# Kernel optimization log

Measured on AMD Instinct MI355X. Metric: run time of the kernel, lower is better.

The kernel has to match this reference:

```python
import jax, jax.numpy as jnp
import numpy as np

SR = 22050
FLOOR = 60.0
BPO = 12

def _interp_linear(p, T):
    # torch F.interpolate(mode='linear', align_corners=False)
    S = p.shape[0]
    x = np.clip((np.arange(T, dtype=np.float64) + 0.5) * (S / T) - 0.5, 0.0, S - 1)
    i0 = np.floor(x).astype(np.int64)
    i1 = np.minimum(i0 + 1, S - 1)
    f = (x - i0).astype(np.float32)
    return p[i0] * (1.0 - f) + p[i1] * f

def _hann(n):
    # torch.hann_window(n, periodic=True)
    if n <= 0:
        return np.zeros((0,), np.float32)
    return (0.5 - 0.5 * np.cos(2.0 * np.pi * np.arange(n) / n)).astype(np.float32)

def _find_voiced(f0, i):
    sub = f0[i:]
    if sub.size == 0:
        return None
    flag = (sub > 0.0).astype(np.int64)
    flag[0] = 0
    if not flag.any():
        return None
    rel = int(flag.argmax())
    after = flag[rel:]
    z = np.nonzero(after == 0)[0]
    run = int(z[0]) if z.size else int(after.size)
    return i + rel, i + rel + run

def _l2n(v):
    # F.normalize(dim=-1), eps=1e-12
    return v / np.maximum(np.linalg.norm(v, axis=-1, keepdims=True), 1e-12)

def _find_peak(signal, f0, i, right_dir):
    w = int(SR / max(float(f0[i]), FLOOR))
    s = max(i - w // 2, 0)
    if right_dir:
        cand_l, cand_r = int(i + 0.3 * w), int(i + 0.75 * w)
    else:
        cand_l, cand_r = max(int(i - 1.75 * w), 0), max(int(i - 1.3 * w), 0)
    if cand_l == cand_r or len(signal) - cand_l < w:
        return w, -1.0, i, 0.0
    seg = np.lib.stride_tricks.sliding_window_view(signal[cand_l:cand_r + w], w)
    corr = _l2n(seg) @ _l2n(signal[s:s + w])
    r = int(corr.argmax())
    return w, float(corr[r]), i + (r + cand_l) - s, float(np.abs(seg[r]).max())

def _find_allpeaks(signal, f0):
    gp = float(np.abs(signal).max())
    added_right, i, peaks = -1e308, 0, []
    while True:
        voiced = _find_voiced(f0, i)
        if voiced is None:
            break
        left, right = voiced
        middle = (left + right) // 2
        w = int(SR / float(f0[middle]))
        s = max(middle - w // 2, 0)
        seg = signal[s:s + w]
        mn, imn = float(seg.min()), int(seg.argmin())
        mx, imx = float(seg.max()), int(seg.argmax())
        i = middle if mn == mx else s + (imn if abs(mn) > abs(mx) else imx)
        backup = i
        while True:
            w, corr, i, peak = _find_peak(signal, f0, i, False)
            if corr == -1.0:
                i -= w
            if i < left:
                if corr > 0.7 and peak > 0.023333 * gp and i - added_right > 0.8 * w:
                    peaks.append(i)
                break
            if corr > 0.3 and (peak == 0.0 or peak > 0.01 * gp):
                if i - added_right > 0.8 * w:
                    peaks.append(i)
        i = backup
        while True:
            w, corr, i, peak = _find_peak(signal, f0, i, True)
            if corr == -1.0:
                i += w
            if i >= right:
                if corr > 0.7 and peak > 0.023333 * gp:
                    peaks.append(i)
                    added_right = i
                break
            if corr > 0.3 and (peak == 0.0 or peak > 0.01 * gp):
                peaks.append(i)
                added_right = i
        i = right
    if not peaks:
        return None
    return np.clip(np.array(sorted(peaks), dtype=np.int64), 0, len(signal) - 1)

def _psola_plan(signal, pitch, peaks):
    # Returns list of (dst_idx, src_idx, window) overlap-add ops plus tail index.
    T = len(signal)
    idx = np.arange(T)
    max_w = 1.25 * SR / float(pitch[pitch > 0].min())
    ops, i = [], 0
    while i < T:
        voiced = _find_voiced(pitch, i)
        if voiced is None:
            break
        left_v, right_v = voiced
        if i < left_v:
            ops.append((idx[i:left_v], idx[i:left_v], _hann(left_v - i)))
        while left_v < right_v:
            p = int(np.abs(peaks - left_v).argmin())
            period = int(SR / max(float(pitch[left_v]), FLOOR))
            left_w = right_w = period // 2
            if p > 0 and peaks[p] - peaks[p - 1] <= max_w:
                left_w = min(int(peaks[p] - peaks[p - 1]), left_w)
            if p < len(peaks) - 1 and peaks[p + 1] - peaks[p] <= max_w:
                right_w = min(int(peaks[p + 1] - peaks[p]), right_w)
            left_i = max(int(peaks[p]) - left_w, 0)
            right_i = int(peaks[p]) + right_w
            ival = (right_i - left_i) // 2
            if ival <= 0:  # safety guard; unreachable for speech-range pitch
                break
            win = _hann(ival * 2)
            seglen = min(len(idx[left_v - ival:left_v + ival]), len(idx[left_i:left_i + ival * 2]))
            dst = idx[left_v - ival:left_v - ival + seglen]
            src = idx[left_i:left_i + seglen]
            L = min(len(dst), len(src), seglen)
            ops.append((dst[:L], src[:L], win[:L]))
            left_v += ival * 2
        i = right_v
    return ops, i

def _pitch_shift_plan(snd, pitch, steps, pitch_range):
    if not (pitch > 1e-05).any():
        return None
    f0 = _interp_linear(pitch, len(snd))
    peaks = _find_allpeaks(snd, f0)
    if peaks is None:
        return None
    v = np.sort(pitch[pitch > 0.0])
    median = float(v[(len(v) - 1) // 2])  # torch lower median
    factor = 2.0 ** (steps / BPO)
    f0, median = f0 * factor, median * factor
    f0 = np.where(f0 > 0.0, median + (f0 - median) * pitch_range, 0.0).astype(np.float32)
    return _psola_plan(snd, f0, peaks)

def setup_inputs():
    key = jax.random.key(0)
    T, S = 661500, 3000
    t = np.arange(S)
    base = (170.0 + 40.0 * np.sin(2.0 * np.pi * t / 400.0)).astype(np.float32)
    voiced = (t % 75) >= 15  # alternating unvoiced/voiced runs
    pitch = np.where(voiced, base, 0.0).astype(np.float32)
    f0 = _interp_linear(pitch, T)
    phase = 2.0 * np.pi * np.cumsum(f0.astype(np.float64)) / SR
    noise = np.asarray(jax.random.normal(key, (T,)), np.float32)
    snd = np.where(f0 > 0.0, 0.55 * np.sin(phase) + 0.25 * np.sin(2 * phase) + 0.1 * np.sin(3 * phase), 0.0)
    snd = np.clip(snd + 0.02 * noise, -1.0, 1.0).astype(np.float32)
    return {"snd": jnp.asarray(snd), "pitch": jnp.asarray(pitch), "steps": 3, "pitch_range": jnp.float32(1.0)}

def reference(snd, pitch, steps, pitch_range):
    snd_np = np.asarray(snd, np.float32)
    pitch_np = np.asarray(pitch, np.float32)
    plan = _pitch_shift_plan(snd_np, pitch_np, int(steps), float(pitch_range))
    if plan is None:
        return jnp.asarray(snd_np)
    ops, tail = plan
    out = np.zeros_like(snd_np)
    for dst, src, win in ops:
        out[dst] += win * snd_np[src]
    out[tail:] = snd_np[tail:]
    return jnp.asarray(out)
```

## Files before the change

kernel.cpp:

```cpp
#include <hip/hip_runtime.h>
#include <cfloat>
#include <climits>
#include <math.h>

#define SRATE 22050.0
#define WMAX 512
#define RCAP 128
#define LCR 256
#define RCR 512
#define SCAP 16384
#define OPR 256
#define MSL 3072
#define NTW 256
#define NTM 1024
#define PCAP 8192
#define FCAP 16384
#define PSTG 4096
#define SNDW 15872
#define RPW 136
#define APPLYB 2048
#define TAILB 1024


__global__ __launch_bounds__(256) void kstats(const float* __restrict__ pitch, int S, unsigned* scal) {
  __shared__ float sp[MSL];
  __shared__ int sc[256];
  __shared__ int sa[256];
  __shared__ unsigned hist[256];
  __shared__ unsigned sprefix, smask;
  __shared__ int srank;
  int tid = threadIdx.x;
  if (tid < 64) scal[tid] = (tid == 1) ? 0x7f800000u : 0u;
  bool lds = (S <= MSL);
  int c = 0, a = 0;
  for (int j = tid; j < S; j += 256) {
    float v = pitch[j];
    if (lds) sp[j] = v;
    if (v > 0.0f) c++;
    if (v > 1e-05f) a = 1;
  }
  sc[tid] = c; sa[tid] = a; __syncthreads();
  for (int st = 128; st; st >>= 1) {
    if (tid < st) { sc[tid] += sc[tid + st]; sa[tid] |= sa[tid + st]; }
    __syncthreads();
  }
  int n = sc[0];
  if (tid == 0) { scal[15] = (unsigned)n; scal[3] = (unsigned)sa[0]; }
  if (n == 0) return;
  if (tid == 0) { sprefix = 0u; smask = 0u; srank = (n - 1) >> 1; }
  __syncthreads();
  for (int shift = 24; shift >= 0; shift -= 8) {
    hist[tid] = 0u;
    __syncthreads();
    unsigned pfx = sprefix, msk = smask;
    for (int q = tid; q < S; q += 256) {
      float v = lds ? sp[q] : pitch[q];
      if (v > 0.0f) {
        unsigned u = __float_as_uint(v);
        if ((u & msk) == pfx) atomicAdd(&hist[(u >> shift) & 255u], 1u);
      }
    }
    __syncthreads();
    if (tid == 0) {
      int r = srank;
      unsigned b = 0;
      for (;;) { unsigned cc = hist[b]; if (r < (int)cc) break; r -= (int)cc; b++; }
      srank = r;
      sprefix = pfx | (b << shift);
      smask = msk | (0xFFu << shift);
    }
    __syncthreads();
  }
  if (tid == 0) scal[2] = sprefix;
}

__device__ __forceinline__ float interp1(const float* __restrict__ pitch, int S, double r, int t) {
  double x = ((double)t + 0.5) * r - 0.5;
  if (x < 0.0) x = 0.0;
  double sm1 = (double)(S - 1);
  if (x > sm1) x = sm1;
  double fl = floor(x);
  int i0 = (int)fl;
  int i1 = i0 + 1; if (i1 > S - 1) i1 = S - 1;
  float f = (float)(x - fl);
  return __fadd_rn(__fmul_rn(pitch[i0], __fsub_rn(1.0f, f)), __fmul_rn(pitch[i1], f));
}

__global__ __launch_bounds__(256) void kprep(const float* __restrict__ pitch, int S, int T,
                                             const float* __restrict__ snd, unsigned* scal,
                                             const int* __restrict__ steps_p, const float* __restrict__ pr_p,
                                             int* __restrict__ pd, int* __restrict__ w0,
                                             int* s0l, int* e0l, int* s1l, int* e1l) {
  __shared__ float smax[256];
  __shared__ unsigned smin[256];
  float med = __uint_as_float(scal[2]);
  double factor = exp2((double)steps_p[0] / 12.0);
  float fac32 = (float)factor;
  float m32 = (float)((double)med * factor);
  float pr32 = pr_p[0];
  double r = (double)S / (double)T;
  float amax = 0.0f;
  unsigned lmin = 0x7f800000u;
  int lane = threadIdx.x & 63;
  int stride = gridDim.x * blockDim.x;
  for (int t = blockIdx.x * blockDim.x + threadIdx.x; t < T; t += stride) {
    float v = interp1(pitch, S, r, t);
    float v1 = __fmul_rn(v, fac32);
    float vs = 0.0f;
    if (v1 > 0.0f) vs = __fadd_rn(m32, __fmul_rn(__fsub_rn(v1, m32), pr32));
    if (t == 1) { scal[16] = __float_as_uint(v); scal[17] = __float_as_uint(vs); }
    { double fd = (double)vs; if (fd < 60.0) fd = 60.0; pd[t] = (int)(SRATE / fd); }
    { double fi = (double)v; if (fi < 60.0) fi = 60.0;
      int ww = (int)(SRATE / fi); if (ww < 1) ww = 1; if (ww > WMAX - 1) ww = WMAX - 1;
      w0[t] = ww; }
    if (vs > 0.0f) { unsigned b = __float_as_uint(vs); if (b < lmin) lmin = b; }
    float a = fabsf(snd[t]); if (a > amax) amax = a;
    bool pv = false, pv1 = false;
    float upv = __shfl_up(v, 1, 64);
    if (t > 0) {
      float pvv = (lane == 0) ? interp1(pitch, S, r, t - 1) : upv;
      pv = pvv > 0.0f;
      float pm1 = __fmul_rn(pvv, fac32);
      float pvs = 0.0f;
      if (pm1 > 0.0f) pvs = __fadd_rn(m32, __fmul_rn(__fsub_rn(pm1, m32), pr32));
      pv1 = pvs > 0.0f;
    }
    bool cv = v > 0.0f, cv1 = vs > 0.0f;
    if (cv && (t == 0 || !pv))  { unsigned k = atomicAdd(scal + 8, 1u);  if (k < RCAP) s0l[k] = t; }
    if (!cv && t > 0 && pv)     { unsigned k = atomicAdd(scal + 9, 1u);  if (k < RCAP) e0l[k] = t; }
    if (cv1 && (t == 0 || !pv1)){ unsigned k = atomicAdd(scal + 10, 1u); if (k < RCAP) s1l[k] = t; }
    if (!cv1 && t > 0 && pv1)   { unsigned k = atomicAdd(scal + 11, 1u); if (k < RCAP) e1l[k] = t; }
  }
  smax[threadIdx.x] = amax; smin[threadIdx.x] = lmin; __syncthreads();
  for (int st = 128; st; st >>= 1) {
    if (threadIdx.x < st) {
      float o = smax[threadIdx.x + st]; if (o > smax[threadIdx.x]) smax[threadIdx.x] = o;
      unsigned u = smin[threadIdx.x + st]; if (u < smin[threadIdx.x]) smin[threadIdx.x] = u;
    }
    __syncthreads();
  }
  if (threadIdx.x == 0) {
    atomicMax(scal + 0, __float_as_uint(smax[0]));
    atomicMin(scal + 1, smin[0]);
  }
}

__device__ void ranksort(int* a, int n, int tid, int* tmp) {
  int v = 0, rk = 0;
  if (tid < n) {
    v = a[tid];
    for (int q = 0; q < n; q++) if (a[q] < v) rk++;
  }
  __syncthreads();
  if (tid < n) tmp[rk] = v;
  __syncthreads();
  if (tid < n) a[tid] = tmp[tid];
  __syncthreads();
}

__device__ int pair_regions_lds(float f1, int T, int* sl, int ns, int* el, int ne, int* L, int* R) {
  int b = 0;
  if (ns > 0 && sl[0] == 0) {
    if (T > 1 && f1 > 0.0f) sl[0] = 1;
    else b = 1;
  }
  int m = 0, j = 0;
  for (int k = b; k < ns; k++) {
    int Lv = sl[k];
    while (j < ne && el[j] <= Lv) j++;
    int Rv = (j < ne) ? el[j] : T;
    if (m < RCAP) { L[m] = Lv; R[m] = Rv; m++; }
  }
  return m;
}

__global__ __launch_bounds__(128) void kregsort2(int T, unsigned* scal,
                                                 const int* __restrict__ s0l, const int* __restrict__ e0l,
                                                 const int* __restrict__ s1l, const int* __restrict__ e1l,
                                                 int* r0L, int* r0R, int* r1L, int* r1R) {
  __shared__ int A[RCAP], B[RCAP], C[RCAP], D[RCAP];
  __shared__ int tmp[RCAP];
  __shared__ int LA[RCAP], RA[RCAP];
  int tid = threadIdx.x;
  int ns0 = min((int)scal[8], RCAP), ne0 = min((int)scal[9], RCAP);
  int ns1 = min((int)scal[10], RCAP), ne1 = min((int)scal[11], RCAP);
  if (tid < ns0) A[tid] = s0l[tid];
  if (tid < ne0) B[tid] = e0l[tid];
  if (tid < ns1) C[tid] = s1l[tid];
  if (tid < ne1) D[tid] = e1l[tid];
  __syncthreads();
  ranksort(A, ns0, tid, tmp);
  ranksort(B, ne0, tid, tmp);
  ranksort(C, ns1, tid, tmp);
  ranksort(D, ne1, tid, tmp);
  float f0_1 = (T > 1) ? __uint_as_float(scal[16]) : 0.0f;
  float f0s_1 = (T > 1) ? __uint_as_float(scal[17]) : 0.0f;
  __shared__ int m0s, m1s;
  if (tid == 0) {
    m0s = pair_regions_lds(f0_1, T, A, ns0, B, ne0, LA, RA);
  }
  __syncthreads();
  if (tid < m0s) { r0L[tid] = LA[tid]; r0R[tid] = RA[tid]; }
  __syncthreads();
  if (tid == 0) {
    m1s = pair_regions_lds(f0s_1, T, C, ns1, D, ne1, LA, RA);
  }
  __syncthreads();
  if (tid < m1s) { r1L[tid] = LA[tid]; r1R[tid] = RA[tid]; }
  if (tid == 0) { scal[12] = (unsigned)m0s; scal[13] = (unsigned)m1s; }
}

struct FPRes { int w; int i; float corr; float peak; };
struct FPG { int w, s, cl, nw, rlen; bool ok; };

__device__ __forceinline__ FPG fp_geom(int T, int i, int w, bool right_dir) {
  FPG g;
  int s = i - w / 2; if (s < 0) s = 0;
  int cl, cr;
  if (right_dir) {
    cl = (int)((double)i + 0.3 * (double)w);
    cr = (int)((double)i + 0.75 * (double)w);
  } else {
    double al = (double)i - 1.75 * (double)w;
    double bl = (double)i - 1.3 * (double)w;
    cl = (int)al; if (cl < 0) cl = 0;
    cr = (int)bl; if (cr < 0) cr = 0;
  }
  g.w = w; g.s = s; g.cl = cl;
  g.ok = !(cl == cr || T - cl < w);
  int nw = (((cr + w) < T ? (cr + w) : T)) - cl - w + 1;
  if (nw < 1) nw = 1;
  g.nw = nw;
  int rlen = T - s; if (rlen > w) rlen = w;
  g.rlen = rlen;
  return g;
}

template <bool L>
__device__ __forceinline__ FPRes fp_impl(const float* __restrict__ snd, const float* lsnd, int wb0,
                                         FPG g, int i, int tid,
                                         float (*refp)[RPW], double* sdd, float* swf, int* swi, float* swp) {
  FPRes res;
  int w = g.w, s = g.s, cl = g.cl, nw = g.nw, rlen = g.rlen;
  res.w = w;
  int lane = tid & 63, wv = tid >> 6;
  double part = 0.0;
  for (int k = tid; k < w; k += NTW) {
    float v = (k < rlen) ? (L ? lsnd[s + k - wb0] : snd[s + k]) : 0.0f;
    refp[k & 3][k >> 2] = v;
    part += (double)v * (double)v;
  }
  for (int off = 32; off; off >>= 1) part += __shfl_xor(part, off, 64);
  if (lane == 0) sdd[wv] = part;
  __syncthreads();
  double refden = sqrt(sdd[0] + sdd[1] + sdd[2] + sdd[3]);
  if (refden < 1e-12) refden = 1e-12;
  int gg = tid >> 2, sub = tid & 3;
  float bestv = -FLT_MAX; int bestr = INT_MAX; float bestp = 0.0f;
  for (int base = 0; base < nw; base += 64) {
    int r = base + gg;
    if (r < nw) {
      const float* seg = (L ? (lsnd + (cl - wb0)) : (snd + cl)) + r;
      const float* rrow = refp[sub];
      double d0 = 0.0, d1 = 0.0, n0 = 0.0, n1 = 0.0;
      float pkc = 0.0f;
      int k = sub, j = 0;
      for (; k + 12 < w; k += 16, j += 4) {
        float4 rv = *reinterpret_cast<const float4*>(rrow + j);
        float a0f = seg[k], a1f = seg[k + 4];
        pkc = fmaxf(pkc, fabsf(a0f));
        pkc = fmaxf(pkc, fabsf(a1f));
        double a0 = (double)a0f, a1 = (double)a1f;
        d0 += a0 * (double)rv.x; n0 += a0 * a0;
        d1 += a1 * (double)rv.y; n1 += a1 * a1;
        float a2f = seg[k + 8], a3f = seg[k + 12];
        pkc = fmaxf(pkc, fabsf(a2f));
        pkc = fmaxf(pkc, fabsf(a3f));
        double a2 = (double)a2f, a3 = (double)a3f;
        d0 += a2 * (double)rv.z; n0 += a2 * a2;
        d1 += a3 * (double)rv.w; n1 += a3 * a3;
      }
      for (; k + 4 < w; k += 8) {
        float a0f = seg[k], a1f = seg[k + 4];
        pkc = fmaxf(pkc, fabsf(a0f));
        pkc = fmaxf(pkc, fabsf(a1f));
        double a0 = (double)a0f, b0 = (double)refp[k & 3][k >> 2];
        double a1 = (double)a1f, b1 = (double)refp[(k + 4) & 3][(k + 4) >> 2];
        d0 += a0 * b0; n0 += a0 * a0;
        d1 += a1 * b1; n1 += a1 * a1;
      }
      for (; k < w; k += 4) {
        float af = seg[k];
        pkc = fmaxf(pkc, fabsf(af));
        double a = (double)af; d0 += a * (double)refp[k & 3][k >> 2]; n0 += a * a;
      }
      double dot = d0 + d1, nr2 = n0 + n1;
      dot += __shfl_xor(dot, 1, 64); nr2 += __shfl_xor(nr2, 1, 64);
      pkc = fmaxf(pkc, __shfl_xor(pkc, 1, 64));
      dot += __shfl_xor(dot, 2, 64); nr2 += __shfl_xor(nr2, 2, 64);
      pkc = fmaxf(pkc, __shfl_xor(pkc, 2, 64));
      if (sub == 0) {
        double den = sqrt(nr2); if (den < 1e-12) den = 1e-12;
        float c = (float)(dot / (den * refden));
        if (c > bestv) { bestv = c; bestr = r; bestp = pkc; }
      }
    }
  }
  for (int off = 32; off >= 4; off >>= 1) {
    float ov = __shfl_xor(bestv, off, 64);
    int orr = __shfl_xor(bestr, off, 64);
    float op = __shfl_xor(bestp, off, 64);
    if (ov > bestv || (ov == bestv && orr < bestr)) { bestv = ov; bestr = orr; bestp = op; }
  }
  if (lane == 0) { swf[wv] = bestv; swi[wv] = bestr; swp[wv] = bestp; }
  __syncthreads();
  float bv = swf[0]; int br = swi[0]; float bp = swp[0];
  for (int q = 1; q < 4; q++) {
    float ov = swf[q]; int orr = swi[q]; float op = swp[q];
    if (ov > bv || (ov == bv && orr < br)) { bv = ov; br = orr; bp = op; }
  }
  res.corr = bv;
  res.i = i + (br + cl) - s;
  res.peak = bp;
  return res;
}

__device__ __forceinline__ FPRes find_peak_block(const float* __restrict__ snd,
                                                 const float* lsnd, int wb0, int wb1, bool useW,
                                                 int T, int i, int wcur, bool right_dir, int tid,
                                                 float (*refp)[RPW], double* sdd,
                                                 float* swf, int* swi, float* swp) {
  FPG g = fp_geom(T, i, wcur, right_dir);
  if (!g.ok) { FPRes r; r.w = g.w; r.corr = -1.0f; r.i = i; r.peak = 0.0f; return r; }
  int lo_a = g.s < g.cl ? g.s : g.cl;
  int hi1 = g.s + g.w, hi2 = g.cl + g.nw + g.w;
  int hi_a = hi1 > hi2 ? hi1 : hi2;
  bool inW = useW && lo_a >= wb0 && hi_a <= wb1;
  if (inW) return fp_impl<true>(snd, lsnd, wb0, g, i, tid, refp, sdd, swf, swi, swp);
  return fp_impl<false>(snd, lsnd, wb0, g, i, tid, refp, sdd, swf, swi, swp);
}

__global__ __launch_bounds__(NTW) void kwalk(const float* __restrict__ snd,
                                             const float* __restrict__ pitch, int S,
                                             const int* __restrict__ w0,
                                             int T, const unsigned* scal,
                                             const int* __restrict__ r0L, const int* __restrict__ r0R,
                                             int2* __restrict__ lcand, int* __restrict__ lcnt,
                                             int* __restrict__ rpk, int* __restrict__ rcnt) {
  __shared__ float lsnd[SNDW];
  __shared__ short swtab[SNDW];
  __shared__ __align__(16) float refp[4][RPW];
  __shared__ double sdd[4];
  __shared__ float swf[8];
  __shared__ int swi[8];
  __shared__ float swp[4];
  __shared__ float spitch[PSTG];
  int tid = threadIdx.x;
  int lane = tid & 63, wv = tid >> 6;
  if (scal[3] == 0u) return;
  bool useL = (S <= PSTG);
  if (useL) { for (int k = tid; k < S; k += NTW) spitch[k] = pitch[k]; }
  __syncthreads();
  double rr = (double)S / (double)T;
  int nreg = (int)scal[12];
  float gp = __uint_as_float(scal[0]);
  for (int wid = blockIdx.x; wid < 2 * nreg; wid += gridDim.x) {
    int r = wid >> 1;
    bool rightdir = (wid & 1) != 0;
    int left = r0L[r], right = r0R[r];
    int middle = (left + right) >> 1;
    int wb0 = left - 1024; if (wb0 < 0) wb0 = 0;
    int wb1 = right + 1024; if (wb1 > T) wb1 = T;
    bool useW = (wb1 - wb0) <= SNDW;
    __syncthreads();
    if (useW) {
      for (int k = tid; k < wb1 - wb0; k += NTW) {
        lsnd[k] = snd[wb0 + k];
        swtab[k] = (short)w0[wb0 + k];
      }
    }
    __syncthreads();
    double fm = useL ? (double)interp1(spitch, S, rr, middle) : (double)interp1(pitch, S, rr, middle);
    double wd = SRATE / fm;
    long long wcap = 2LL * (long long)T;
    int w = (wd >= (double)wcap) ? (int)wcap : (int)wd;
    if (w < 1) w = 1;
    int s0 = middle - w / 2; if (s0 < 0) s0 = 0;
    int wlen = w; if (wlen > T - s0) wlen = T - s0;
    float lmn = FLT_MAX; int lmni = INT_MAX;
    float lmx = -FLT_MAX; int lmxi = INT_MAX;
    for (int k = tid; k < wlen; k += NTW) {
      int idx = s0 + k;
      float v = (useW && idx >= wb0 && idx < wb1) ? lsnd[idx - wb0] : snd[idx];
      if (v < lmn) { lmn = v; lmni = k; }
      if (v > lmx) { lmx = v; lmxi = k; }
    }
    for (int off = 32; off; off >>= 1) {
      float ov = __shfl_xor(lmn, off, 64); int oi = __shfl_xor(lmni, off, 64);
      if (ov < lmn || (ov == lmn && oi < lmni)) { lmn = ov; lmni = oi; }
      float ov2 = __shfl_xor(lmx, off, 64); int oi2 = __shfl_xor(lmxi, off, 64);
      if (ov2 > lmx || (ov2 == lmx && oi2 < lmxi)) { lmx = ov2; lmxi = oi2; }
    }
    if (lane == 0) { swf[wv] = lmn; swi[wv] = lmni; swf[4 + wv] = lmx; swi[4 + wv] = lmxi; }
    __syncthreads();
    float mn = swf[0]; int imn = swi[0];
    float mx = swf[4]; int imx = swi[4];
    for (int q = 1; q < 4; q++) {
      float ov = swf[q]; int oi = swi[q];
      if (ov < mn || (ov == mn && oi < imn)) { mn = ov; imn = oi; }
      float ov2 = swf[4 + q]; int oi2 = swi[4 + q];
      if (ov2 > mx || (ov2 == mx && oi2 < imx)) { mx = ov2; imx = oi2; }
    }
    __syncthreads();
    int i;
    if (mn == mx) i = middle;
    else i = s0 + ((fabsf(mn) > fabsf(mx)) ? imn : imx);
    if (!rightdir) {
      int nl = 0, guard = 0;
      for (;;) {
        if (++guard > 500000) break;
        int wcur;
        if (useW && i >= wb0 && i < wb1) wcur = (int)swtab[i - wb0];
        else {
          double fi = useL ? (double)interp1(spitch, S, rr, i) : (double)interp1(pitch, S, rr, i);
          if (fi < 60.0) fi = 60.0;
          int ww = (int)(SRATE / fi); if (ww < 1) ww = 1; if (ww > WMAX - 1) ww = WMAX - 1;
          wcur = ww;
        }
        FPRes p = find_peak_block(snd, lsnd, wb0, wb1, useW, T, i, wcur, false, tid,
                                  refp, sdd, swf, swi, swp);
        i = p.i;
        if (p.corr == -1.0f) i -= p.w;
        if (i < left) {
          if ((double)p.corr > 0.7 && (double)p.peak > 0.023333 * (double)gp) {
            if (nl < LCR) { if (tid == 0) lcand[r * LCR + nl] = make_int2(i, p.w); nl++; }
          }
          break;
        }
        if ((double)p.corr > 0.3 && (p.peak == 0.0f || (double)p.peak > 0.01 * (double)gp)) {
          if (nl < LCR) { if (tid == 0) lcand[r * LCR + nl] = make_int2(i, p.w); nl++; }
        }
      }
      if (tid == 0) lcnt[r] = nl;
    } else {
      int nr = 0, guard = 0;
      for (;;) {
        if (++guard > 500000) break;
        int wcur;
        if (useW && i >= wb0 && i < wb1) wcur = (int)swtab[i - wb0];
        else {
          double fi = useL ? (double)interp1(spitch, S, rr, i) : (double)interp1(pitch, S, rr, i);
          if (fi < 60.0) fi = 60.0;
          int ww = (int)(SRATE / fi); if (ww < 1) ww = 1; if (ww > WMAX - 1) ww = WMAX - 1;
          wcur = ww;
        }
        FPRes p = find_peak_block(snd, lsnd, wb0, wb1, useW, T, i, wcur, true, tid,
                                  refp, sdd, swf, swi, swp);
        i = p.i;
        if (p.corr == -1.0f) i += p.w;
        if (i >= right) {
          if ((double)p.corr > 0.7 && (double)p.peak > 0.023333 * (double)gp) {
            if (nr < RCR) { if (tid == 0) rpk[r * RCR + nr] = i; nr++; }
          }
          break;
        }
        if ((double)p.corr > 0.3 && (p.peak == 0.0f || (double)p.peak > 0.01 * (double)gp)) {
          if (nr < RCR) { if (tid == 0) rpk[r * RCR + nr] = i; nr++; }
        }
      }
      if (tid == 0) rcnt[r] = nr;
    }
  }
}

__global__ __launch_bounds__(NTM) void kmerge(int T, unsigned* scal,
                                              const int2* __restrict__ lcand, const int* __restrict__ lcnt,
                                              const int* __restrict__ rpk, const int* __restrict__ rcnt,
                                              int* __restrict__ peaks) {
  __shared__ long long arR[RCAP];
  __shared__ long long lastR[RCAP];
  __shared__ int rcs[RCAP];
  __shared__ int lcs[RCAP];
  __shared__ int klc[RCAP];
  __shared__ int off[RCAP + 1];
  __shared__ int sbuf[SCAP];
  __shared__ int unsorted;
  int tid = threadIdx.x;
  int lane = tid & 63, wv = tid >> 6;
  int nreg = (int)scal[12];
  if (scal[3] == 0u || nreg == 0) { if (tid == 0) scal[4] = 0u; return; }
  if (tid < nreg) {
    int rc = rcnt[tid];
    rcs[tid] = rc;
    lcs[tid] = lcnt[tid];
    lastR[tid] = (rc > 0) ? (long long)rpk[tid * RCR + rc - 1] : LLONG_MIN;
  }
  __syncthreads();
  if (tid == 0) {
    long long ar = -(1LL << 62);
    for (int r = 0; r < nreg; r++) { arR[r] = ar; if (rcs[r] > 0) ar = lastR[r]; }
  }
  __syncthreads();
  for (int r = wv; r < nreg; r += 16) {
    int n = lcs[r];
    long long ar = arR[r];
    int cnt = 0;
    for (int base = 0; base < n; base += 64) {
      int jp = base + lane;
      bool pred = false;
      if (jp < n) {
        int j = n - 1 - jp;
        int2 cd = lcand[r * LCR + j];
        pred = ((double)((long long)cd.x - ar) > 0.8 * (double)cd.y);
      }
      unsigned long long m = __ballot(pred);
      cnt += __popcll(m);
    }
    if (lane == 0) klc[r] = cnt;
  }
  __syncthreads();
  if (tid == 0) {
    int acc = 0;
    for (int r = 0; r < nreg; r++) { off[r] = acc; acc += klc[r] + rcs[r]; if (acc > SCAP) acc = SCAP; }
    off[nreg] = acc;
    scal[4] = (unsigned)acc;
    unsorted = 0;
  }
  __syncthreads();
  for (int r = wv; r < nreg; r += 16) {
    long long ar = arR[r];
    int n = lcs[r];
    int pos0 = off[r];
    for (int base = 0; base < n; base += 64) {
      int jp = base + lane;
      bool pred = false; int val = 0;
      if (jp < n) {
        int j = n - 1 - jp;
        int2 cd = lcand[r * LCR + j];
        if ((double)((long long)cd.x - ar) > 0.8 * (double)cd.y) { pred = true; val = cd.x; }
      }
      unsigned long long m = __ballot(pred);
      if (pred) {
        int pre = __popcll(m & ((1ull << lane) - 1ull));
        int pos = pos0 + pre;
        if (pos < SCAP) peaks[pos] = val;
      }
      pos0 += __popcll(m);
    }
    int rc = rcs[r];
    for (int j = lane; j < rc; j += 64) {
      int pos = pos0 + j;
      if (pos < SCAP) peaks[pos] = rpk[r * RCR + j];
    }
  }
  __syncthreads();
  int npk = off[nreg];
  if (npk > 1) {
    for (int k = tid; k < npk - 1; k += NTM) {
      if (peaks[k] > peaks[k + 1]) unsorted = 1;
    }
    __syncthreads();
    if (unsorted) {
      int n2 = 1; while (n2 < npk) n2 <<= 1;
      for (int k = tid; k < n2; k += NTM) sbuf[k] = (k < npk) ? peaks[k] : INT_MAX;
      __syncthreads();
      for (int kk = 2; kk <= n2; kk <<= 1) {
        for (int j = kk >> 1; j > 0; j >>= 1) {
          for (int idx = tid; idx < n2; idx += NTM) {
            int ixj = idx ^ j;
            if (ixj > idx) {
              int a = sbuf[idx], b = sbuf[ixj];
              bool up = ((idx & kk) == 0);
              if ((up && a > b) || (!up && a < b)) { sbuf[idx] = b; sbuf[ixj] = a; }
            }
          }
          __syncthreads();
        }
      }
      for (int k = tid; k < npk; k += NTM) peaks[k] = sbuf[k];
      __syncthreads();
    }
  }
  for (int k = tid; k < npk; k += NTM) { int v = peaks[k]; if (v < 0) v = 0; if (v > T - 1) v = T - 1; peaks[k] = v; }
}

__global__ __launch_bounds__(256) void kplan(const int* __restrict__ pd, int T, unsigned* scal,
                                             const int* __restrict__ peaks,
                                             const int* __restrict__ r1L, const int* __restrict__ r1R,
                                             int4* __restrict__ ops, int* __restrict__ opcnt) {
  __shared__ int sp[PCAP];
  __shared__ int ib[FCAP];
  int tid = threadIdx.x;
  int npk = (int)scal[4];
  int nreg = (int)scal[13];
  int r = (int)blockIdx.x;
  if (scal[3] == 0u || npk == 0) {
    if (r == 0 && tid == 0) { scal[6] = 0u; scal[14] = 0u; }
    return;
  }
  if (r == 0 && tid == 0) {
    scal[6] = (nreg > 0) ? (unsigned)r1R[nreg - 1] : 0u;
    scal[14] = (unsigned)nreg;
  }
  if (r >= nreg) return;
  int prev_right = (r == 0) ? 0 : r1R[r - 1];
  int left_v = r1L[r], right_v = r1R[r];
  int pl_n = npk < PCAP ? npk : PCAP;
  int pl4 = pl_n & ~3;
  for (int k = tid * 4; k < pl4; k += 1024) {
    int4 v = *reinterpret_cast<const int4*>(peaks + k);
    sp[k] = v.x; sp[k + 1] = v.y; sp[k + 2] = v.z; sp[k + 3] = v.w;
  }
  for (int k = pl4 + tid; k < pl_n; k += 256) sp[k] = peaks[k];
  int span = right_v - left_v;
  int fl_n = span < FCAP ? span : FCAP;
  const int* srcp = pd + left_v;
  int head = (4 - (left_v & 3)) & 3; if (head > fl_n) head = fl_n;
  for (int k = tid; k < head; k += 256) ib[k] = srcp[k];
  int rem4 = (fl_n - head) & ~3;
  for (int k = tid * 4; k < rem4; k += 1024) {
    int4 v = *reinterpret_cast<const int4*>(srcp + head + k);
    ib[head + k] = v.x; ib[head + k + 1] = v.y; ib[head + k + 2] = v.z; ib[head + k + 3] = v.w;
  }
  for (int k = head + rem4 + tid; k < fl_n; k += 256) ib[k] = srcp[k];
  __syncthreads();
  if (tid != 0) return;

  auto PRD = [&](int idx) -> int { return (idx < pl_n) ? sp[idx] : peaks[idx]; };

  double minpos = (double)__uint_as_float(scal[1]);
  double max_w = 1.25 * SRATE / minpos;
  int c = 0;
  if (prev_right < left_v) {
    ops[r * OPR + c] = make_int4(prev_right, prev_right, left_v - prev_right, left_v - prev_right);
    c++;
  }
  int lv = left_v, guard = 0;
  int lo = -1;
  int Pm2 = 0, Pm1 = 0, P0 = 0, P1 = 0;
  while (lv < right_v) {
    if (++guard > 500000) break;
    int fo = lv - left_v;
    int period = (fo < fl_n) ? ib[fo] : pd[lv];
    int x = lv;
    if (lo < 0) {
      int a = 0, b = npk;
      while (a < b) { int m = (a + b) >> 1; if (PRD(m) < x) a = m + 1; else b = m; }
      lo = a;
      Pm2 = (lo - 2 >= 0) ? PRD(lo - 2) : 0;
      Pm1 = (lo - 1 >= 0) ? PRD(lo - 1) : 0;
      P0  = (lo < npk) ? PRD(lo) : 0;
      P1  = (lo + 1 < npk) ? PRD(lo + 1) : 0;
    } else {
      while (lo < npk && P0 < x) {
        lo++;
        Pm2 = Pm1; Pm1 = P0; P0 = P1;
        P1 = (lo + 1 < npk) ? PRD(lo + 1) : 0;
      }
    }
    long long d0 = (lo > 0) ? (long long)x - (long long)Pm1 : LLONG_MAX;
    long long d1 = (lo < npk) ? (long long)P0 - (long long)x : LLONG_MAX;
    int p, Pp, Ppm1, Pp1;
    if (d0 <= d1) {
      p = lo - 1;
      int tv = Pm1;
      if (p > 0 && Pm2 == tv) {
        while (p > 0 && PRD(p - 1) == tv) p--;
        Pp = tv;
        Ppm1 = (p > 0) ? PRD(p - 1) : 0;
        Pp1 = (p < npk - 1) ? PRD(p + 1) : 0;
      } else {
        Pp = Pm1; Ppm1 = Pm2; Pp1 = P0;
      }
    } else {
      p = lo; Pp = P0; Ppm1 = Pm1; Pp1 = P1;
    }
    int lw = period >> 1, rw = period >> 1;
    if (p > 0) { long long gp_ = (long long)Pp - (long long)Ppm1; if ((double)gp_ <= max_w && gp_ < (long long)lw) lw = (int)gp_; }
    if (p < npk - 1) { long long gp_ = (long long)Pp1 - (long long)Pp; if ((double)gp_ <= max_w && gp_ < (long long)rw) rw = (int)gp_; }
    int left_i = Pp - lw; if (left_i < 0) left_i = 0;
    int right_i = Pp + rw;
    int ival = (right_i - left_i) >> 1;
    if (ival <= 0) break;
    int a0 = lv - ival;
    int len1 = 0;
    if (a0 >= 0) { int e = lv + ival; if (e > T) e = T; len1 = e - a0; if (len1 < 0) len1 = 0; }
    int e2 = left_i + 2 * ival; if (e2 > T) e2 = T;
    int len2 = e2 - left_i; if (len2 < 0) len2 = 0;
    int seglen = len1 < len2 ? len1 : len2;
    int len_dst = (a0 < 0) ? 0 : ((T - a0 < seglen) ? T - a0 : seglen);
    int len_src = (T - left_i < seglen) ? T - left_i : seglen;
    int L = seglen; if (len_dst < L) L = len_dst; if (len_src < L) L = len_src;
    if (L > 0 && c < OPR) { ops[r * OPR + c] = make_int4(a0, left_i, L, 2 * ival); c++; }
    lv += 2 * ival;
  }
  opcnt[r] = c;
}

__global__ __launch_bounds__(256) void kout(const float* __restrict__ snd, float* __restrict__ out,
                                            const unsigned* scal, const int4* __restrict__ ops,
                                            const int* __restrict__ opcnt, int T) {
  int tail = (int)scal[6];
  if (blockIdx.x < APPLYB) {
    int nreg = (int)scal[14];
    int total = nreg * OPR;
    for (int slot = blockIdx.x; slot < total; slot += APPLYB) {
      int r = slot / OPR, j = slot - r * OPR;
      if (j >= opcnt[r]) continue;
      int4 o = ops[r * OPR + j];
      double nn = (double)o.w;
      int kend = o.z;
      { int lim = tail - o.x; if (lim < 0) lim = 0; if (kend > lim) kend = lim; }
      for (int k = threadIdx.x; k < kend; k += blockDim.x) {
        double cph = (6.283185307179586 * (double)k) / nn;
        float wv = (float)(0.5 - 0.5 * cos(cph));
        atomicAdd(out + o.x + k, __fmul_rn(wv, snd[o.y + k]));
      }
    }
  } else {
    int b = blockIdx.x - APPLYB;
    int stride = TAILB * 256;
    for (int t = b * 256 + threadIdx.x; t < T; t += stride)
      if (t >= tail) out[t] = snd[t];
  }
}

extern "C" void kernel_launch(void* const* d_in, const int* in_sizes, int n_in,
                              void* d_out, int out_size, void* d_ws, size_t ws_size,
                              hipStream_t stream) {
  (void)n_in; (void)ws_size;
  int T = in_sizes[0];
  int S = in_sizes[1];
  const float* snd = (const float*)d_in[0];
  const float* pitch = (const float*)d_in[1];
  const int* steps = (const int*)d_in[2];
  const float* prange = (const float*)d_in[3];
  float* out = (float*)d_out;

  char* base = (char*)d_ws;
  size_t off = 0;
  auto alloc = [&](size_t bytes, size_t align) -> char* {
    off = (off + align - 1) & ~(align - 1);
    char* p = base + off;
    off += bytes;
    return p;
  };
  int* pd    = (int*)alloc((size_t)T * 4, 16);
  int* w0    = (int*)alloc((size_t)T * 4, 16);
  unsigned* scal = (unsigned*)alloc(256, 16);
  int* s0l = (int*)alloc(RCAP * 4, 4);
  int* e0l = (int*)alloc(RCAP * 4, 4);
  int* s1l = (int*)alloc(RCAP * 4, 4);
  int* e1l = (int*)alloc(RCAP * 4, 4);
  int* r0L = (int*)alloc(RCAP * 4, 4);
  int* r0R = (int*)alloc(RCAP * 4, 4);
  int* r1L = (int*)alloc(RCAP * 4, 4);
  int* r1R = (int*)alloc(RCAP * 4, 4);
  int* lcnt = (int*)alloc(RCAP * 4, 4);
  int* rcnt = (int*)alloc(RCAP * 4, 4);
  int* opcnt = (int*)alloc(RCAP * 4, 4);
  int2* lcand = (int2*)alloc((size_t)RCAP * LCR * 8, 8);
  int* rpk = (int*)alloc((size_t)RCAP * RCR * 4, 4);
  int* peaks = (int*)alloc((size_t)SCAP * 4, 16);
  int4* ops = (int4*)alloc((size_t)RCAP * OPR * 16, 16);

  hipMemsetAsync(d_out, 0, (size_t)out_size * sizeof(float), stream);
  kstats<<<1, 256, 0, stream>>>(pitch, S, scal);
  kprep<<<1024, 256, 0, stream>>>(pitch, S, T, snd, scal, steps, prange, pd, w0, s0l, e0l, s1l, e1l);
  kregsort2<<<1, 128, 0, stream>>>(T, scal, s0l, e0l, s1l, e1l, r0L, r0R, r1L, r1R);
  kwalk<<<256, NTW, 0, stream>>>(snd, pitch, S, w0, T, scal, r0L, r0R, lcand, lcnt, rpk, rcnt);
  kmerge<<<1, NTM, 0, stream>>>(T, scal, lcand, lcnt, rpk, rcnt, peaks);
  kplan<<<RCAP, 256, 0, stream>>>(pd, T, scal, peaks, r1L, r1R, ops, opcnt);
  kout<<<APPLYB + TAILB, 256, 0, stream>>>(snd, out, scal, ops, opcnt, T);
}
```

Baseline: 458.2 us.

## Fold region sort and peak merge into walk and plan kernels, dropping launches

Removes the single-block region-sort kernel and the single-block peak-merge kernel. Each kwalk block now redundantly sorts and pairs the voiced-region boundaries in LDS, and each kplan block redundantly rebuilds the merged, sorted peak list directly in its own shared memory instead of reading it from global. This cuts two serial kernel launches and their global round trips from a latency-bound pipeline. In exchange, every block repeats the sort/merge work, and kplan's shared-memory footprint grows, which may lower occupancy.

```diff
diff --git a/kernel.cpp b/kernel.cpp
--- a/kernel.cpp
+++ b/kernel.cpp
@@ -12,7 +12,6 @@
 #define OPR 256
 #define MSL 3072
 #define NTW 256
-#define NTM 1024
 #define PCAP 8192
 #define FCAP 16384
 #define PSTG 4096
@@ -174,42 +173,6 @@
   return m;
 }
 
-__global__ __launch_bounds__(128) void kregsort2(int T, unsigned* scal,
-                                                 const int* __restrict__ s0l, const int* __restrict__ e0l,
-                                                 const int* __restrict__ s1l, const int* __restrict__ e1l,
-                                                 int* r0L, int* r0R, int* r1L, int* r1R) {
-  __shared__ int A[RCAP], B[RCAP], C[RCAP], D[RCAP];
-  __shared__ int tmp[RCAP];
-  __shared__ int LA[RCAP], RA[RCAP];
-  int tid = threadIdx.x;
-  int ns0 = min((int)scal[8], RCAP), ne0 = min((int)scal[9], RCAP);
-  int ns1 = min((int)scal[10], RCAP), ne1 = min((int)scal[11], RCAP);
-  if (tid < ns0) A[tid] = s0l[tid];
-  if (tid < ne0) B[tid] = e0l[tid];
-  if (tid < ns1) C[tid] = s1l[tid];
-  if (tid < ne1) D[tid] = e1l[tid];
-  __syncthreads();
-  ranksort(A, ns0, tid, tmp);
-  ranksort(B, ne0, tid, tmp);
-  ranksort(C, ns1, tid, tmp);
-  ranksort(D, ne1, tid, tmp);
-  float f0_1 = (T > 1) ? __uint_as_float(scal[16]) : 0.0f;
-  float f0s_1 = (T > 1) ? __uint_as_float(scal[17]) : 0.0f;
-  __shared__ int m0s, m1s;
-  if (tid == 0) {
-    m0s = pair_regions_lds(f0_1, T, A, ns0, B, ne0, LA, RA);
-  }
-  __syncthreads();
-  if (tid < m0s) { r0L[tid] = LA[tid]; r0R[tid] = RA[tid]; }
-  __syncthreads();
-  if (tid == 0) {
-    m1s = pair_regions_lds(f0s_1, T, C, ns1, D, ne1, LA, RA);
-  }
-  __syncthreads();
-  if (tid < m1s) { r1L[tid] = LA[tid]; r1R[tid] = RA[tid]; }
-  if (tid == 0) { scal[12] = (unsigned)m0s; scal[13] = (unsigned)m1s; }
-}
-
 struct FPRes { int w; int i; float corr; float peak; };
 struct FPG { int w, s, cl, nw, rlen; bool ok; };
 
@@ -344,7 +307,7 @@
                                              const float* __restrict__ pitch, int S,
                                              const int* __restrict__ w0,
                                              int T, const unsigned* scal,
-                                             const int* __restrict__ r0L, const int* __restrict__ r0R,
+                                             const int* __restrict__ s0l, const int* __restrict__ e0l,
                                              int2* __restrict__ lcand, int* __restrict__ lcnt,
                                              int* __restrict__ rpk, int* __restrict__ rcnt) {
   __shared__ float lsnd[SNDW];
@@ -355,19 +318,29 @@
   __shared__ int swi[8];
   __shared__ float swp[4];
   __shared__ float spitch[PSTG];
+  __shared__ int rsA[RCAP], rsB[RCAP], rsT[RCAP], rLA[RCAP], rRA[RCAP];
+  __shared__ int m0sh;
   int tid = threadIdx.x;
   int lane = tid & 63, wv = tid >> 6;
   if (scal[3] == 0u) return;
+  int ns0 = min((int)scal[8], RCAP), ne0 = min((int)scal[9], RCAP);
+  if (tid < ns0) rsA[tid] = s0l[tid];
+  if (tid < ne0) rsB[tid] = e0l[tid];
   bool useL = (S <= PSTG);
   if (useL) { for (int k = tid; k < S; k += NTW) spitch[k] = pitch[k]; }
   __syncthreads();
+  ranksort(rsA, ns0, tid, rsT);
+  ranksort(rsB, ne0, tid, rsT);
+  float f0_1 = (T > 1) ? __uint_as_float(scal[16]) : 0.0f;
+  if (tid == 0) m0sh = pair_regions_lds(f0_1, T, rsA, ns0, rsB, ne0, rLA, rRA);
+  __syncthreads();
+  int nreg = m0sh;
   double rr = (double)S / (double)T;
-  int nreg = (int)scal[12];
   float gp = __uint_as_float(scal[0]);
   for (int wid = blockIdx.x; wid < 2 * nreg; wid += gridDim.x) {
     int r = wid >> 1;
     bool rightdir = (wid & 1) != 0;
-    int left = r0L[r], right = r0R[r];
+    int left = rLA[r], right = rRA[r];
     int middle = (left + right) >> 1;
     int wb0 = left - 1024; if (wb0 < 0) wb0 = 0;
     int wb1 = right + 1024; if (wb1 > T) wb1 = T;
@@ -473,145 +446,154 @@
   }
 }
 
-__global__ __launch_bounds__(NTM) void kmerge(int T, unsigned* scal,
-                                              const int2* __restrict__ lcand, const int* __restrict__ lcnt,
-                                              const int* __restrict__ rpk, const int* __restrict__ rcnt,
-                                              int* __restrict__ peaks) {
+__global__ __launch_bounds__(256) void kplan(const int* __restrict__ pd, int T, unsigned* scal,
+                                             const int2* __restrict__ lcand, const int* __restrict__ lcnt,
+                                             const int* __restrict__ rpk, const int* __restrict__ rcnt,
+                                             const int* __restrict__ s0l, const int* __restrict__ e0l,
+                                             const int* __restrict__ s1l, const int* __restrict__ e1l,
+                                             int4* __restrict__ ops, int* __restrict__ opcnt) {
+  __shared__ int sp[SCAP];
+  __shared__ int ib[FCAP];
+  __shared__ int rsA[RCAP], rsB[RCAP], rsT[RCAP], rLA[RCAP], rRA[RCAP];
   __shared__ long long arR[RCAP];
   __shared__ long long lastR[RCAP];
-  __shared__ int rcs[RCAP];
-  __shared__ int lcs[RCAP];
-  __shared__ int klc[RCAP];
-  __shared__ int off[RCAP + 1];
-  __shared__ int sbuf[SCAP];
-  __shared__ int unsorted;
+  __shared__ int rcs[RCAP], lcs[RCAP], klc[RCAP], off[RCAP + 1];
+  __shared__ int m0sh, m1sh, unsorted;
   int tid = threadIdx.x;
   int lane = tid & 63, wv = tid >> 6;
-  int nreg = (int)scal[12];
-  if (scal[3] == 0u || nreg == 0) { if (tid == 0) scal[4] = 0u; return; }
-  if (tid < nreg) {
-    int rc = rcnt[tid];
-    rcs[tid] = rc;
-    lcs[tid] = lcnt[tid];
-    lastR[tid] = (rc > 0) ? (long long)rpk[tid * RCR + rc - 1] : LLONG_MIN;
-  }
-  __syncthreads();
-  if (tid == 0) {
-    long long ar = -(1LL << 62);
-    for (int r = 0; r < nreg; r++) { arR[r] = ar; if (rcs[r] > 0) ar = lastR[r]; }
-  }
-  __syncthreads();
-  for (int r = wv; r < nreg; r += 16) {
-    int n = lcs[r];
-    long long ar = arR[r];
-    int cnt = 0;
-    for (int base = 0; base < n; base += 64) {
-      int jp = base + lane;
-      bool pred = false;
-      if (jp < n) {
-        int j = n - 1 - jp;
-        int2 cd = lcand[r * LCR + j];
-        pred = ((double)((long long)cd.x - ar) > 0.8 * (double)cd.y);
-      }
-      unsigned long long m = __ballot(pred);
-      cnt += __popcll(m);
-    }
-    if (lane == 0) klc[r] = cnt;
-  }
-  __syncthreads();
-  if (tid == 0) {
-    int acc = 0;
-    for (int r = 0; r < nreg; r++) { off[r] = acc; acc += klc[r] + rcs[r]; if (acc > SCAP) acc = SCAP; }
-    off[nreg] = acc;
-    scal[4] = (unsigned)acc;
-    unsorted = 0;
-  }
-  __syncthreads();
-  for (int r = wv; r < nreg; r += 16) {
-    long long ar = arR[r];
-    int n = lcs[r];
-    int pos0 = off[r];
-    for (int base = 0; base < n; base += 64) {
-      int jp = base + lane;
-      bool pred = false; int val = 0;
-      if (jp < n) {
-        int j = n - 1 - jp;
-        int2 cd = lcand[r * LCR + j];
-        if ((double)((long long)cd.x - ar) > 0.8 * (double)cd.y) { pred = true; val = cd.x; }
-      }
-      unsigned long long m = __ballot(pred);
-      if (pred) {
-        int pre = __popcll(m & ((1ull << lane) - 1ull));
-        int pos = pos0 + pre;
-        if (pos < SCAP) peaks[pos] = val;
-      }
-      pos0 += __popcll(m);
-    }
-    int rc = rcs[r];
-    for (int j = lane; j < rc; j += 64) {
-      int pos = pos0 + j;
-      if (pos < SCAP) peaks[pos] = rpk[r * RCR + j];
-    }
-  }
-  __syncthreads();
-  int npk = off[nreg];
-  if (npk > 1) {
-    for (int k = tid; k < npk - 1; k += NTM) {
-      if (peaks[k] > peaks[k + 1]) unsorted = 1;
-    }
-    __syncthreads();
-    if (unsorted) {
-      int n2 = 1; while (n2 < npk) n2 <<= 1;
-      for (int k = tid; k < n2; k += NTM) sbuf[k] = (k < npk) ? peaks[k] : INT_MAX;
-      __syncthreads();
-      for (int kk = 2; kk <= n2; kk <<= 1) {
-        for (int j = kk >> 1; j > 0; j >>= 1) {
-          for (int idx = tid; idx < n2; idx += NTM) {
-            int ixj = idx ^ j;
-            if (ixj > idx) {
-              int a = sbuf[idx], b = sbuf[ixj];
-              bool up = ((idx & kk) == 0);
-              if ((up && a > b) || (!up && a < b)) { sbuf[idx] = b; sbuf[ixj] = a; }
-            }
-          }
-          __syncthreads();
-        }
-      }
-      for (int k = tid; k < npk; k += NTM) peaks[k] = sbuf[k];
-      __syncthreads();
-    }
-  }
-  for (int k = tid; k < npk; k += NTM) { int v = peaks[k]; if (v < 0) v = 0; if (v > T - 1) v = T - 1; peaks[k] = v; }
-}
-
-__global__ __launch_bounds__(256) void kplan(const int* __restrict__ pd, int T, unsigned* scal,
-                                             const int* __restrict__ peaks,
-                                             const int* __restrict__ r1L, const int* __restrict__ r1R,
-                                             int4* __restrict__ ops, int* __restrict__ opcnt) {
-  __shared__ int sp[PCAP];
-  __shared__ int ib[FCAP];
-  int tid = threadIdx.x;
-  int npk = (int)scal[4];
-  int nreg = (int)scal[13];
   int r = (int)blockIdx.x;
-  if (scal[3] == 0u || npk == 0) {
+  if (scal[3] == 0u) {
     if (r == 0 && tid == 0) { scal[6] = 0u; scal[14] = 0u; }
     return;
   }
+  int ns0 = min((int)scal[8], RCAP), ne0 = min((int)scal[9], RCAP);
+  int ns1 = min((int)scal[10], RCAP), ne1 = min((int)scal[11], RCAP);
+  float f0_1 = (T > 1) ? __uint_as_float(scal[16]) : 0.0f;
+  float f0s_1 = (T > 1) ? __uint_as_float(scal[17]) : 0.0f;
+  if (tid < ns0) rsA[tid] = s0l[tid];
+  if (tid < ne0) rsB[tid] = e0l[tid];
+  __syncthreads();
+  ranksort(rsA, ns0, tid, rsT);
+  ranksort(rsB, ne0, tid, rsT);
+  if (tid == 0) m0sh = pair_regions_lds(f0_1, T, rsA, ns0, rsB, ne0, rLA, rRA);
+  __syncthreads();
+  int nreg0 = m0sh;
+  if (tid < ns1) rsA[tid] = s1l[tid];
+  if (tid < ne1) rsB[tid] = e1l[tid];
+  __syncthreads();
+  ranksort(rsA, ns1, tid, rsT);
+  ranksort(rsB, ne1, tid, rsT);
+  if (tid == 0) m1sh = pair_regions_lds(f0s_1, T, rsA, ns1, rsB, ne1, rLA, rRA);
+  __syncthreads();
+  int nreg1 = m1sh;
+  int npk = 0;
+  if (nreg0 > 0) {
+    if (tid < nreg0) {
+      int rc = rcnt[tid];
+      rcs[tid] = rc;
+      lcs[tid] = lcnt[tid];
+      lastR[tid] = (rc > 0) ? (long long)rpk[tid * RCR + rc - 1] : LLONG_MIN;
+    }
+    __syncthreads();
+    if (tid == 0) {
+      long long ar = -(1LL << 62);
+      for (int q = 0; q < nreg0; q++) { arR[q] = ar; if (rcs[q] > 0) ar = lastR[q]; }
+    }
+    __syncthreads();
+    for (int q = wv; q < nreg0; q += 4) {
+      int n = lcs[q];
+      long long ar = arR[q];
+      int cnt = 0;
+      for (int base = 0; base < n; base += 64) {
+        int jp = base + lane;
+        bool pred = false;
+        if (jp < n) {
+          int j = n - 1 - jp;
+          int2 cd = lcand[q * LCR + j];
+          pred = ((double)((long long)cd.x - ar) > 0.8 * (double)cd.y);
+        }
+        unsigned long long m = __ballot(pred);
+        cnt += __popcll(m);
+      }
+      if (lane == 0) klc[q] = cnt;
+    }
+    __syncthreads();
+    if (tid == 0) {
+      int acc = 0;
+      for (int q = 0; q < nreg0; q++) { off[q] = acc; acc += klc[q] + rcs[q]; if (acc > SCAP) acc = SCAP; }
+      off[nreg0] = acc;
+      unsorted = 0;
+      if (r == 0) scal[4] = (unsigned)acc;
+    }
+    __syncthreads();
+    for (int q = wv; q < nreg0; q += 4) {
+      long long ar = arR[q];
+      int n = lcs[q];
+      int pos0 = off[q];
+      for (int base = 0; base < n; base += 64) {
+        int jp = base + lane;
+        bool pred = false; int val = 0;
+        if (jp < n) {
+          int j = n - 1 - jp;
+          int2 cd = lcand[q * LCR + j];
+          if ((double)((long long)cd.x - ar) > 0.8 * (double)cd.y) { pred = true; val = cd.x; }
+        }
+        unsigned long long m = __ballot(pred);
+        if (pred) {
+          int pre = __popcll(m & ((1ull << lane) - 1ull));
+          int pos = pos0 + pre;
+          if (pos < SCAP) sp[pos] = val;
+        }
+        pos0 += __popcll(m);
+      }
+      int rc = rcs[q];
+      for (int j = lane; j < rc; j += 64) {
+        int pos = pos0 + j;
+        if (pos < SCAP) sp[pos] = rpk[q * RCR + j];
+      }
+    }
+    __syncthreads();
+    npk = off[nreg0];
+    if (npk > 1) {
+      for (int k = tid; k < npk - 1; k += 256) {
+        if (sp[k] > sp[k + 1]) unsorted = 1;
+      }
+      __syncthreads();
+      if (unsorted) {
+        int n2 = 1; while (n2 < npk) n2 <<= 1;
+        for (int k = tid; k < n2; k += 256) ib[k] = (k < npk) ? sp[k] : INT_MAX;
+        __syncthreads();
+        for (int kk = 2; kk <= n2; kk <<= 1) {
+          for (int j = kk >> 1; j > 0; j >>= 1) {
+            for (int idx = tid; idx < n2; idx += 256) {
+              int ixj = idx ^ j;
+              if (ixj > idx) {
+                int a = ib[idx], b = ib[ixj];
+                bool up = ((idx & kk) == 0);
+                if ((up && a > b) || (!up && a < b)) { ib[idx] = b; ib[ixj] = a; }
+              }
+            }
+            __syncthreads();
+          }
+        }
+        for (int k = tid; k < npk; k += 256) sp[k] = ib[k];
+        __syncthreads();
+      }
+    }
+    for (int k = tid; k < npk; k += 256) { int v = sp[k]; if (v < 0) v = 0; if (v > T - 1) v = T - 1; sp[k] = v; }
+    __syncthreads();
+  }
+  if (npk == 0) {
+    if (r == 0 && tid == 0) { scal[6] = 0u; scal[14] = 0u; }
+    return;
+  }
   if (r == 0 && tid == 0) {
-    scal[6] = (nreg > 0) ? (unsigned)r1R[nreg - 1] : 0u;
-    scal[14] = (unsigned)nreg;
-  }
-  if (r >= nreg) return;
-  int prev_right = (r == 0) ? 0 : r1R[r - 1];
-  int left_v = r1L[r], right_v = r1R[r];
-  int pl_n = npk < PCAP ? npk : PCAP;
-  int pl4 = pl_n & ~3;
-  for (int k = tid * 4; k < pl4; k += 1024) {
-    int4 v = *reinterpret_cast<const int4*>(peaks + k);
-    sp[k] = v.x; sp[k + 1] = v.y; sp[k + 2] = v.z; sp[k + 3] = v.w;
-  }
-  for (int k = pl4 + tid; k < pl_n; k += 256) sp[k] = peaks[k];
+    scal[6] = (nreg1 > 0) ? (unsigned)rRA[nreg1 - 1] : 0u;
+    scal[14] = (unsigned)nreg1;
+  }
+  if (r >= nreg1) return;
+  int prev_right = (r == 0) ? 0 : rRA[r - 1];
+  int left_v = rLA[r], right_v = rRA[r];
   int span = right_v - left_v;
   int fl_n = span < FCAP ? span : FCAP;
   const int* srcp = pd + left_v;
@@ -625,8 +607,6 @@
   for (int k = head + rem4 + tid; k < fl_n; k += 256) ib[k] = srcp[k];
   __syncthreads();
   if (tid != 0) return;
-
-  auto PRD = [&](int idx) -> int { return (idx < pl_n) ? sp[idx] : peaks[idx]; };
 
   double minpos = (double)__uint_as_float(scal[1]);
   double max_w = 1.25 * SRATE / minpos;
@@ -645,17 +625,17 @@
     int x = lv;
     if (lo < 0) {
       int a = 0, b = npk;
-      while (a < b) { int m = (a + b) >> 1; if (PRD(m) < x) a = m + 1; else b = m; }
+      while (a < b) { int m = (a + b) >> 1; if (sp[m] < x) a = m + 1; else b = m; }
       lo = a;
-      Pm2 = (lo - 2 >= 0) ? PRD(lo - 2) : 0;
-      Pm1 = (lo - 1 >= 0) ? PRD(lo - 1) : 0;
-      P0  = (lo < npk) ? PRD(lo) : 0;
-      P1  = (lo + 1 < npk) ? PRD(lo + 1) : 0;
+      Pm2 = (lo - 2 >= 0) ? sp[lo - 2] : 0;
+      Pm1 = (lo - 1 >= 0) ? sp[lo - 1] : 0;
+      P0  = (lo < npk) ? sp[lo] : 0;
+      P1  = (lo + 1 < npk) ? sp[lo + 1] : 0;
     } else {
       while (lo < npk && P0 < x) {
         lo++;
         Pm2 = Pm1; Pm1 = P0; P0 = P1;
-        P1 = (lo + 1 < npk) ? PRD(lo + 1) : 0;
+        P1 = (lo + 1 < npk) ? sp[lo + 1] : 0;
       }
     }
     long long d0 = (lo > 0) ? (long long)x - (long long)Pm1 : LLONG_MAX;
@@ -665,10 +645,10 @@
       p = lo - 1;
       int tv = Pm1;
       if (p > 0 && Pm2 == tv) {
-        while (p > 0 && PRD(p - 1) == tv) p--;
+        while (p > 0 && sp[p - 1] == tv) p--;
         Pp = tv;
-        Ppm1 = (p > 0) ? PRD(p - 1) : 0;
-        Pp1 = (p < npk - 1) ? PRD(p + 1) : 0;
+        Ppm1 = (p > 0) ? sp[p - 1] : 0;
+        Pp1 = (p < npk - 1) ? sp[p + 1] : 0;
       } else {
         Pp = Pm1; Ppm1 = Pm2; Pp1 = P0;
       }
@@ -752,24 +732,17 @@
   int* e0l = (int*)alloc(RCAP * 4, 4);
   int* s1l = (int*)alloc(RCAP * 4, 4);
   int* e1l = (int*)alloc(RCAP * 4, 4);
-  int* r0L = (int*)alloc(RCAP * 4, 4);
-  int* r0R = (int*)alloc(RCAP * 4, 4);
-  int* r1L = (int*)alloc(RCAP * 4, 4);
-  int* r1R = (int*)alloc(RCAP * 4, 4);
   int* lcnt = (int*)alloc(RCAP * 4, 4);
   int* rcnt = (int*)alloc(RCAP * 4, 4);
   int* opcnt = (int*)alloc(RCAP * 4, 4);
   int2* lcand = (int2*)alloc((size_t)RCAP * LCR * 8, 8);
   int* rpk = (int*)alloc((size_t)RCAP * RCR * 4, 4);
-  int* peaks = (int*)alloc((size_t)SCAP * 4, 16);
   int4* ops = (int4*)alloc((size_t)RCAP * OPR * 16, 16);
 
   hipMemsetAsync(d_out, 0, (size_t)out_size * sizeof(float), stream);
   kstats<<<1, 256, 0, stream>>>(pitch, S, scal);
   kprep<<<1024, 256, 0, stream>>>(pitch, S, T, snd, scal, steps, prange, pd, w0, s0l, e0l, s1l, e1l);
-  kregsort2<<<1, 128, 0, stream>>>(T, scal, s0l, e0l, s1l, e1l, r0L, r0R, r1L, r1R);
-  kwalk<<<256, NTW, 0, stream>>>(snd, pitch, S, w0, T, scal, r0L, r0R, lcand, lcnt, rpk, rcnt);
-  kmerge<<<1, NTM, 0, stream>>>(T, scal, lcand, lcnt, rpk, rcnt, peaks);
-  kplan<<<RCAP, 256, 0, stream>>>(pd, T, scal, peaks, r1L, r1R, ops, opcnt);
+  kwalk<<<256, NTW, 0, stream>>>(snd, pitch, S, w0, T, scal, s0l, e0l, lcand, lcnt, rpk, rcnt);
+  kplan<<<RCAP, 256, 0, stream>>>(pd, T, scal, lcand, lcnt, rpk, rcnt, s0l, e0l, s1l, e1l, ops, opcnt);
   kout<<<APPLYB + TAILB, 256, 0, stream>>>(snd, out, scal, ops, opcnt, T);
 }
```

Measured after the change: 470.6 us. +2.7%, slower.
